# Kernel optimization log

Measured on AMD Instinct MI355X. Metric: run time of the kernel, lower is better.

The kernel has to match this reference:

```python
import jax, jax.numpy as jnp
import numpy as np

H = 16  # n_heads
D = 64  # d_keys


def setup_inputs() -> dict:
    key = jax.random.key(0)
    ks = jax.random.split(key, 11)
    b, n, dm = 2, 2048, 1024
    s = 1.0 / np.sqrt(dm)
    return {
        "q": jax.random.normal(ks[0], (b, n, dm), jnp.float32),
        "k": jax.random.normal(ks[1], (b, n, dm), jnp.float32),
        "v": jax.random.normal(ks[2], (b, n, dm), jnp.float32),
        "Wq": jax.random.normal(ks[3], (dm, H * D), jnp.float32) * s,
        "bq": jax.random.normal(ks[4], (H * D,), jnp.float32) * 0.01,
        "Wk": jax.random.normal(ks[5], (dm, H * D), jnp.float32) * s,
        "bk": jax.random.normal(ks[6], (H * D,), jnp.float32) * 0.01,
        "Wv": jax.random.normal(ks[7], (dm, H * D), jnp.float32) * s,
        "bv": jax.random.normal(ks[8], (H * D,), jnp.float32) * 0.01,
        "Wo": jax.random.normal(ks[9], (H * D, dm), jnp.float32) * s,
        "bo": jax.random.normal(ks[10], (dm,), jnp.float32) * 0.01,
    }


def reference(q, k, v, Wq, bq, Wk, bk, Wv, bv, Wo, bo):
    b, n_q, _ = q.shape
    n_k = k.shape[1]
    # projections -> [b, n, h, d]
    qh = (q @ Wq + bq).reshape(b, n_q, H, D)
    kh = (k @ Wk + bk).reshape(b, n_k, H, D)
    vh = (v @ Wv + bv).reshape(b, n_k, H, D)
    # scores [b, h, n, m]
    scores = jnp.einsum('bnhd,bmhd->bhnm', qh, kh)
    causal = jnp.triu(jnp.ones((n_q, n_k), dtype=bool), k=1)  # True above diag
    scores = jnp.where(causal, -jnp.inf, scores)
    att = jax.nn.softmax(scores / np.sqrt(D).astype(np.float32), axis=-1)
    att_out = jnp.einsum('bhnm,bmhd->bnhd', att, vh).reshape(b, n_q, H * D)
    return att_out @ Wo + bo
```

## Files before the change

kernel.cpp:

```cpp
#include <hip/hip_runtime.h>

typedef float f32x4 __attribute__((ext_vector_type(4)));
typedef __bf16 bf16x8 __attribute__((ext_vector_type(8)));
typedef __bf16 bf16x4 __attribute__((ext_vector_type(4)));
typedef __bf16 bf16_t;

#define NH 16
#define DH 64
#define SEQ 2048
#define DM 1024

#define QSCALE 0.18033688f

extern "C" hipError_t hipMemPtrGetInfo(void* ptr, size_t* size);

__device__ __forceinline__ bf16x8 ld8(const bf16_t* p) { return *(const bf16x8*)p; }
__device__ __forceinline__ void st8(bf16_t* p, bf16x8 v) { *(bf16x8*)p = v; }

__device__ __forceinline__ void gl_lds16(const bf16_t* g, bf16_t* l)
{
    __builtin_amdgcn_global_load_lds(
        (const __attribute__((address_space(1))) unsigned int*)g,
        (__attribute__((address_space(3))) unsigned int*)l, 16, 0, 0);
}

__global__ __launch_bounds__(256) void fill_sentinel(float* out, unsigned n, float val)
{
    unsigned stride = gridDim.x * blockDim.x;
    for (unsigned i = blockIdx.x * blockDim.x + threadIdx.x; i < n; i += stride)
        out[i] = val;
}

__global__ __launch_bounds__(256) void prep(
    const float* __restrict__ q, const float* __restrict__ k,
    const float* __restrict__ v,
    const float* __restrict__ w0, const float* __restrict__ w1,
    const float* __restrict__ w2, const float* __restrict__ w3,
    bf16_t* __restrict__ xb, bf16_t* __restrict__ wt, int fragmode)
{
    int z = blockIdx.z;
    if (z < 3) {
        const float* src = (z == 0) ? q : (z == 1) ? k : v;
        bf16_t* dst = xb + (size_t)z * (4096u * 1024u);
        size_t i8 = ((size_t)blockIdx.x * 256 + threadIdx.x) * 8;
        f32x4 u = *(const f32x4*)(src + i8);
        f32x4 w = *(const f32x4*)(src + i8 + 4);
        bf16x8 h = { (bf16_t)u.x, (bf16_t)u.y, (bf16_t)u.z, (bf16_t)u.w,
                     (bf16_t)w.x, (bf16_t)w.y, (bf16_t)w.z, (bf16_t)w.w };
        st8(dst + i8, h);
    } else {
        int x = blockIdx.x;
        if (x >= 1024) return;
        int w = x >> 8, rem = x & 255;
        int bx = rem & 15, by = rem >> 4;
        const float* in = (w == 0) ? w0 : (w == 1) ? w1 : (w == 2) ? w2 : w3;
        bf16_t* out = wt + (size_t)w * DM * DM;
        __shared__ __align__(16) bf16_t tile[64][72];
        int t = threadIdx.x;
        int k0 = by * 64, n0 = bx * 64;
        int r0 = t >> 4, c0 = (t & 15) * 4;
        for (int p = 0; p < 4; p++) {
            int r = r0 + p * 16;
            const float* src = in + (size_t)(k0 + r) * DM + n0 + c0;
            for (int i = 0; i < 4; i++) tile[r][c0 + i] = (bf16_t)src[i];
        }
        __syncthreads();
        if (fragmode && w < 3) {
            int idx = t;
            #pragma unroll
            for (int p = 0; p < 2; p++, idx += 256) {
                int rn = idx & 63;
                int kc8 = idx >> 6;
                int n_abs = n0 + rn;
                int rblk = n_abs >> 4, l16v = n_abs & 15;
                int kk = kc8 >> 2, gg = kc8 & 3;
                bf16x8 vv;
                for (int j = 0; j < 8; j++) vv[j] = tile[kc8 * 8 + j][rn];
                st8(out + (size_t)((rblk * 16 + by) * 2 + kk) * 512
                        + (gg * 16 + l16v) * 8, vv);
            }
        } else {
            for (int p = 0; p < 4; p++) {
                int rn = r0 + p * 16;
                bf16_t* dst = out + (size_t)(n0 + rn) * DM + k0 + c0;
                for (int i = 0; i < 4; i++) dst[i] = tile[c0 + i][rn];
            }
        }
    }
}

#define LGKM0 asm volatile("s_waitcnt lgkmcnt(0)" ::: "memory")
#define VMC(n) asm volatile("s_waitcnt vmcnt(" #n ")" ::: "memory")
#define BARRIER __builtin_amdgcn_s_barrier()

#define STA(d, h, dk) do { \
    _Pragma("unroll") for (int j = 0; j < 2; j++) \
        gl_lds16(Xp + ((h) * 128 + j * 64) * DM + (dk) * 64, \
                 Ab + sdst0 + ((d) * 2 + (h)) * 8192 + j * 4096); } while (0)
#define RDA(d, h, F) do { \
    _Pragma("unroll") for (int mf = 0; mf < 4; mf++) { \
        F[mf][0] = ld8(Ab + rA0 + ((d) * 2 + (h)) * 8192 + mf * 1024); \
        F[mf][1] = ld8(Ab + rA1 + ((d) * 2 + (h)) * 8192 + mf * 1024); } } while (0)
#define LDB(SET, nh, kto) do { \
    _Pragma("unroll") for (int nf = 0; nf < 2; nf++) \
        _Pragma("unroll") for (int kk = 0; kk < 2; kk++) \
            SET[nf][kk] = ld8(Bp + (nh) * 131072 + nf * 16384 \
                              + (kto) * 1024 + kk * 512); } while (0)
#define MMQ(AF, BF, Q) do { \
    __builtin_amdgcn_s_setprio(1); \
    _Pragma("unroll") for (int mf = 0; mf < 4; mf++) \
        _Pragma("unroll") for (int nf = 0; nf < 2; nf++) { \
            Q[mf][nf] = __builtin_amdgcn_mfma_f32_16x16x32_bf16( \
                AF[mf][0], BF[nf][0], Q[mf][nf], 0, 0, 0); \
            Q[mf][nf] = __builtin_amdgcn_mfma_f32_16x16x32_bf16( \
                AF[mf][1], BF[nf][1], Q[mf][nf], 0, 0, 0); } \
    __builtin_amdgcn_s_setprio(0); } while (0)

__global__ __launch_bounds__(512, 2) void gemm8(
    const bf16_t* __restrict__ xall, const bf16_t* __restrict__ bfall,
    const float* __restrict__ b0v, const float* __restrict__ b1v,
    const float* __restrict__ b2v, bf16_t* __restrict__ outall)
{
    int z = blockIdx.z;
    int mode = z;
    const bf16_t* X  = xall  + (size_t)z * (4096u * 1024u);
    const bf16_t* Bf = bfall + (size_t)z * (1024u * 1024u);
    const float* bias = (z == 0) ? b0v : (z == 1) ? b1v : b2v;
    bf16_t* out = outall + (size_t)z * (4096u * 1024u);

    int m0 = blockIdx.x * 256;
    int n0 = blockIdx.y * 256;

    __shared__ __align__(16) bf16_t Ab[2 * 2 * 128 * 64];

    int tid  = threadIdx.x;
    int lane = tid & 63, w = tid >> 6;
    int g = lane >> 4, l16 = lane & 15;
    int wm = w >> 2, wn = w & 3;
    int rl = lane >> 3, cl = lane & 7;
    int w8 = w * 8;

    int srow = w8 + rl;
    int scol = (cl ^ rl) * 8;
    const bf16_t* Xp = X + (size_t)(m0 + srow) * DM + scol;
    int sdst0 = w8 * 64 + lane * 8;

    int x7 = l16 & 7;
    int rA0 = (wm * 64 + l16) * 64 + ((0 + g) ^ x7) * 8;
    int rA1 = (wm * 64 + l16) * 64 + ((4 + g) ^ x7) * 8;

    const bf16_t* Bp = Bf + ((size_t)(n0 >> 4) + wn * 2) * 16384 + lane * 8;

    f32x4 a00[4][2] = {}, a01[4][2] = {}, a10[4][2] = {}, a11[4][2] = {};
    bf16x8 afA[4][2], afB[4][2], Ba[2][2], Bb[2][2];

    STA(0, 0, 0); STA(0, 1, 0); STA(1, 0, 1); STA(1, 1, 1);
    LDB(Ba, 0, 0); LDB(Bb, 1, 0);
    VMC(0);
    BARRIER;
    RDA(0, 0, afA);

    #pragma unroll 1
    for (int i = 0; i < 7; i++) {
        VMC(6); LGKM0; MMQ(afA, Ba, a00); BARRIER;
        STA(0, 0, 2); VMC(4); RDA(0, 1, afB); MMQ(afA, Bb, a01); BARRIER;
        LGKM0; MMQ(afB, Ba, a10); LDB(Ba, 0, 1); BARRIER;
        MMQ(afB, Bb, a11); LDB(Bb, 1, 1); STA(0, 1, 2); RDA(1, 0, afA); BARRIER;
        VMC(6); LGKM0; MMQ(afA, Ba, a00); BARRIER;
        STA(1, 0, 3); VMC(4); RDA(1, 1, afB); MMQ(afA, Bb, a01); BARRIER;
        LGKM0; MMQ(afB, Ba, a10); LDB(Ba, 0, 2); BARRIER;
        MMQ(afB, Bb, a11); LDB(Bb, 1, 2); STA(1, 1, 3); RDA(0, 0, afA); BARRIER;
        Xp += 128; Bp += 2048;
    }
    VMC(6); LGKM0; MMQ(afA, Ba, a00); BARRIER;
    VMC(2); RDA(0, 1, afB); MMQ(afA, Bb, a01); BARRIER;
    LGKM0; MMQ(afB, Ba, a10); LDB(Ba, 0, 1); BARRIER;
    MMQ(afB, Bb, a11); LDB(Bb, 1, 1); RDA(1, 0, afA); BARRIER;
    VMC(4); LGKM0; MMQ(afA, Ba, a00); BARRIER;
    VMC(0); RDA(1, 1, afB); MMQ(afA, Bb, a01); BARRIER;
    LGKM0; MMQ(afB, Ba, a10); BARRIER;
    MMQ(afB, Bb, a11);

    float scale = (mode == 0) ? QSCALE : 1.0f;
#define EPI(Q, Mh, Nh) do { \
    _Pragma("unroll") for (int mf = 0; mf < 4; mf++) { \
        int mbase = m0 + (Mh) * 128 + wm * 64 + mf * 16 + g * 4; \
        int bb = mbase >> 11, nn0 = mbase & 2047; \
        _Pragma("unroll") for (int nf = 0; nf < 2; nf++) { \
            int col = n0 + (Nh) * 128 + wn * 32 + nf * 16 + l16; \
            float bv = bias[col]; \
            int hh = col >> 6, dd = col & 63; \
            if (mode == 2) { \
                bf16x4 pv; \
                for (int r = 0; r < 4; r++) pv[r] = (bf16_t)(Q[mf][nf][r] + bv); \
                *(bf16x4*)(out + ((size_t)(bb * NH + hh) * DH + dd) * SEQ + nn0) = pv; \
            } else { \
                for (int r = 0; r < 4; r++) \
                    out[((size_t)(bb * NH + hh) * SEQ + nn0 + r) * DH + dd] = \
                        (bf16_t)((Q[mf][nf][r] + bv) * scale); \
            } } } } while (0)
    EPI(a00, 0, 0); EPI(a01, 0, 1); EPI(a10, 1, 0); EPI(a11, 1, 1);
#undef EPI
}

__global__ __launch_bounds__(256) void gemm_out(
    const bf16_t* __restrict__ X, const bf16_t* __restrict__ WT,
    const float* __restrict__ bias, bf16_t* __restrict__ out,
    float* __restrict__ outf, int out_is_f32)
{
    int m0 = blockIdx.x * 128;
    int n0 = blockIdx.y * 128;

    __shared__ __align__(16) bf16_t Alds[128 * 64];
    __shared__ __align__(16) bf16_t Blds[128 * 64];

    int t = threadIdx.x;
    int lane = t & 63, wave = t >> 6;
    int g = lane >> 4, l16 = lane & 15;
    int wr0 = (wave >> 1) * 64, wc0 = (wave & 1) * 64;
    int crow = lane >> 3;
    int ccol = (lane & 7) * 8;

    f32x4 acc[4][4] = {};

    for (int k0 = 0; k0 < DM; k0 += 64) {
        __syncthreads();
        for (int c = wave; c < 16; c += 4) {
            int row = c * 8 + crow;
            gl_lds16(X  + (size_t)(m0 + row) * DM + k0 + ccol,
                     Alds + c * 512 + lane * 8);
            gl_lds16(WT + (size_t)(n0 + row) * DM + k0 + ccol,
                     Blds + c * 512 + lane * 8);
        }
        __syncthreads();
        for (int kk = 0; kk < 2; kk++) {
            bf16x8 af[4], bfr[4];
            for (int i = 0; i < 4; i++)
                af[i] = ld8(Alds + (wr0 + i * 16 + l16) * 64 + kk * 32 + g * 8);
            for (int i = 0; i < 4; i++)
                bfr[i] = ld8(Blds + (wc0 + i * 16 + l16) * 64 + kk * 32 + g * 8);
            for (int mi = 0; mi < 4; mi++)
                for (int ni = 0; ni < 4; ni++)
                    acc[mi][ni] = __builtin_amdgcn_mfma_f32_16x16x32_bf16(
                        af[mi], bfr[ni], acc[mi][ni], 0, 0, 0);
        }
    }
    for (int mi = 0; mi < 4; mi++) {
        int mbase = m0 + wr0 + mi * 16 + g * 4;
        for (int ni = 0; ni < 4; ni++) {
            int col = n0 + wc0 + ni * 16 + l16;
            float bv = bias[col];
            for (int r = 0; r < 4; r++) {
                float sv = acc[mi][ni][r] + bv;
                if (out_is_f32) outf[(size_t)(mbase + r) * 1024 + col] = sv;
                else            out[(size_t)(mbase + r) * 1024 + col] = (bf16_t)sv;
            }
        }
    }
}

__global__ __launch_bounds__(256) void gemm_mha(
    const float* __restrict__ x0, const float* __restrict__ x1,
    const float* __restrict__ x2, const bf16_t* __restrict__ xb,
    const bf16_t* __restrict__ wt_base,
    const float* __restrict__ b0, const float* __restrict__ b1,
    const float* __restrict__ b2, bf16_t* __restrict__ out_base,
    float* __restrict__ outf, int mode_base, int out_is_f32)
{
    int z = blockIdx.z;
    const float* Xf    = (z == 0) ? x0 : (z == 1) ? x1 : x2;
    const bf16_t* WT   = wt_base + (size_t)z * DM * DM;
    const float* bias  = (z == 0) ? b0 : (z == 1) ? b1 : b2;
    bf16_t* out = out_base + (size_t)z * (4096u * 1024u);
    int mode = mode_base + z;

    int m0 = blockIdx.x * 128;
    int n0 = blockIdx.y * 128;

    __shared__ __align__(16) bf16_t Alds[128 * 64];
    __shared__ __align__(16) bf16_t Blds[128 * 64];

    int t = threadIdx.x;
    int lane = t & 63, wave = t >> 6;
    int g = lane >> 4, l16 = lane & 15;
    int wr0 = (wave >> 1) * 64, wc0 = (wave & 1) * 64;

    f32x4 acc[4][4] = {};
    int srow = t >> 3, sk = (t & 7) * 8;

    for (int k0 = 0; k0 < DM; k0 += 64) {
        __syncthreads();
        if (mode < 3) {
            for (int p = 0; p < 4; p++) {
                int r = srow + p * 32;
                const float* s4 = Xf + (size_t)(m0 + r) * DM + k0 + sk;
                f32x4 u = *(const f32x4*)s4;
                f32x4 w = *(const f32x4*)(s4 + 4);
                bf16x8 h = { (bf16_t)u.x, (bf16_t)u.y, (bf16_t)u.z, (bf16_t)u.w,
                             (bf16_t)w.x, (bf16_t)w.y, (bf16_t)w.z, (bf16_t)w.w };
                st8(Alds + r * 64 + sk, h);
            }
        } else {
            for (int p = 0; p < 4; p++) {
                int r = srow + p * 32;
                st8(Alds + r * 64 + sk, ld8(xb + (size_t)(m0 + r) * DM + k0 + sk));
            }
        }
        for (int p = 0; p < 4; p++) {
            int r = srow + p * 32;
            st8(Blds + r * 64 + sk, ld8(WT + (size_t)(n0 + r) * DM + k0 + sk));
        }
        __syncthreads();
        for (int kk = 0; kk < 2; kk++) {
            bf16x8 af[4], bfr[4];
            for (int i = 0; i < 4; i++)
                af[i] = ld8(Alds + (wr0 + i * 16 + l16) * 64 + kk * 32 + g * 8);
            for (int i = 0; i < 4; i++)
                bfr[i] = ld8(Blds + (wc0 + i * 16 + l16) * 64 + kk * 32 + g * 8);
            for (int mi = 0; mi < 4; mi++)
                for (int ni = 0; ni < 4; ni++)
                    acc[mi][ni] = __builtin_amdgcn_mfma_f32_16x16x32_bf16(
                        af[mi], bfr[ni], acc[mi][ni], 0, 0, 0);
        }
    }
    float scale = (mode == 0) ? QSCALE : 1.0f;
    for (int mi = 0; mi < 4; mi++) {
        int mbase = m0 + wr0 + mi * 16 + g * 4;
        for (int ni = 0; ni < 4; ni++) {
            int col = n0 + wc0 + ni * 16 + l16;
            float bv = bias[col];
            if (mode == 2) {
                int bb = mbase >> 11, nn0 = mbase & 2047;
                int h = col >> 6, d = col & 63;
                bf16x4 pv;
                for (int r = 0; r < 4; r++) pv[r] = (bf16_t)(acc[mi][ni][r] + bv);
                *(bf16x4*)(out + ((size_t)(bb * NH + h) * DH + d) * SEQ + nn0) = pv;
            } else {
                for (int r = 0; r < 4; r++) {
                    int mr = mbase + r;
                    float sv = (acc[mi][ni][r] + bv) * scale;
                    if (mode == 3) {
                        if (out_is_f32) outf[(size_t)mr * 1024 + col] = sv;
                        else            out[(size_t)mr * 1024 + col] = (bf16_t)sv;
                    } else {
                        int bb = mr >> 11, nn = mr & 2047;
                        int h = col >> 6, d = col & 63;
                        out[((size_t)(bb * NH + h) * SEQ + nn) * DH + d] = (bf16_t)sv;
                    }
                }
            }
        }
    }
}

__constant__ unsigned char JP[24] = {7,15,15,14,14,6,13,13,12,12,5,11,
                                     11,10,10,4,9,9,8,8,3,2,1,0};
__constant__ unsigned char JS[24] = {0,0,1,0,1,0,0,1,0,1,0,0,
                                     1,0,1,0,0,1,0,1,0,0,0,0};

__global__ __launch_bounds__(512) void attn_split(
    const bf16_t* __restrict__ Qh, const bf16_t* __restrict__ Kh,
    const bf16_t* __restrict__ VT, bf16_t* __restrict__ att,
    float* __restrict__ Pb, float* __restrict__ Lb)
{
    int bhx = blockIdx.x;
    int y   = blockIdx.y;
    int p   = JP[y];
    int seg = JS[y];
    bool splitf = (p >= 8);
    int k0 = splitf ? seg * (p + 1) : 0;
    int k1 = splitf ? k0 + (p + 1) : 2 * p + 2;

    const bf16_t* Qb = Qh + (size_t)bhx * SEQ * DH;
    const bf16_t* Kb = Kh + (size_t)bhx * SEQ * DH;
    const bf16_t* Vb = VT + (size_t)bhx * DH * SEQ;

    __shared__ __align__(16) bf16_t Klds[64 * 72];
    __shared__ __align__(16) bf16_t Vlds[64 * 72];
    __shared__ __align__(16) bf16_t Plds[8][16 * 72];

    int t = threadIdx.x, lane = t & 63, wave = t >> 6;
    int g = lane >> 4, l16 = lane & 15;
    int srow = t >> 3, sk = (t & 7) * 8;
    int qt = 2 * p + (wave >> 2);
    int Tw = qt + 1;
    int rowl = (wave & 3) * 16 + l16;

    bf16x8 qf[2];
    for (int kk = 0; kk < 2; kk++)
        qf[kk] = ld8(Qb + (size_t)(qt * 64 + rowl) * DH + kk * 32 + g * 8);

    f32x4 accO[4] = {};
    float l = 0.f;
    bf16_t* Pw = Plds[wave];

    bf16x8 kreg = ld8(Kb + (size_t)(k0 * 64 + srow) * DH + sk);
    bf16x8 vreg = ld8(Vb + (size_t)srow * SEQ + k0 * 64 + sk);
    st8(&Klds[srow * 72 + sk], kreg);
    if (k0 + 1 < k1)
        kreg = ld8(Kb + (size_t)((k0 + 1) * 64 + srow) * DH + sk);

    for (int j = k0; j < k1; j++) {
        __syncthreads();
        st8(&Vlds[srow * 72 + sk], vreg);
        if (j + 1 < k1)
            vreg = ld8(Vb + (size_t)srow * SEQ + (j + 1) * 64 + sk);

        bool act  = (j < Tw);
        bool diag = (j == Tw - 1);
        if (act) {
            f32x4 s[4];
            __builtin_amdgcn_s_setprio(1);
            for (int c = 0; c < 4; c++) {
                f32x4 a = {};
                for (int kk = 0; kk < 2; kk++) {
                    bf16x8 kf = ld8(&Klds[(c * 16 + l16) * 72 + kk * 32 + g * 8]);
                    a = __builtin_amdgcn_mfma_f32_16x16x32_bf16(kf, qf[kk], a, 0, 0, 0);
                }
                s[c] = a;
            }
            __builtin_amdgcn_s_setprio(0);
            for (int c = 0; c < 4; c++) {
                bf16x4 pv;
                for (int r = 0; r < 4; r++) {
                    float v = s[c][r];
                    if (diag && (c * 16 + g * 4 + r) > rowl) v = -1e30f;
                    float pe;
                    asm("v_exp_f32 %0, %1" : "=v"(pe) : "v"(v));
                    l += pe;
                    pv[r] = (bf16_t)pe;
                }
                *(bf16x4*)(Pw + l16 * 72 + c * 16 + g * 4) = pv;
            }
        }
        __syncthreads();
        if (j + 1 < k1) {
            st8(&Klds[srow * 72 + sk], kreg);
            if (j + 2 < k1)
                kreg = ld8(Kb + (size_t)((j + 2) * 64 + srow) * DH + sk);
        }
        if (act) {
            bf16x8 pf0 = ld8(Pw + l16 * 72 + g * 8);
            bf16x8 pf1 = ld8(Pw + l16 * 72 + 32 + g * 8);
            __builtin_amdgcn_s_setprio(1);
            for (int c2 = 0; c2 < 4; c2++) {
                bf16x8 vf0 = ld8(&Vlds[(c2 * 16 + l16) * 72 + g * 8]);
                accO[c2] = __builtin_amdgcn_mfma_f32_16x16x32_bf16(vf0, pf0, accO[c2], 0, 0, 0);
                bf16x8 vf1 = ld8(&Vlds[(c2 * 16 + l16) * 72 + 32 + g * 8]);
                accO[c2] = __builtin_amdgcn_mfma_f32_16x16x32_bf16(vf1, pf1, accO[c2], 0, 0, 0);
            }
            __builtin_amdgcn_s_setprio(0);

            if (diag && !splitf) {
                float lt = l;
                lt += __shfl_xor(lt, 16);
                lt += __shfl_xor(lt, 32);
                float inv = 1.f / lt;
                int qabs = qt * 64 + rowl;
                int bb = bhx >> 4, h = bhx & 15;
                for (int c2 = 0; c2 < 4; c2++) {
                    bf16x4 ov;
                    for (int r = 0; r < 4; r++) ov[r] = (bf16_t)(accO[c2][r] * inv);
                    *(bf16x4*)(att + (((size_t)bb * SEQ + qabs) * NH + h) * DH
                               + c2 * 16 + g * 4) = ov;
                }
            }
        }
    }

    if (splitf) {
        float lt = l;
        lt += __shfl_xor(lt, 16);
        lt += __shfl_xor(lt, 32);
        int slot = (bhx * 16 + (qt - 16)) * 2 + seg;
        float* Pp = Pb + (size_t)slot * 4096 + rowl * 64;
        #pragma unroll
        for (int c2 = 0; c2 < 4; c2++)
            *(f32x4*)(Pp + c2 * 16 + g * 4) = accO[c2];
        if (g == 0) Lb[slot * 64 + rowl] = lt;
    }
}

__global__ __launch_bounds__(256) void attn_combine(
    const float* __restrict__ Pb, const float* __restrict__ Lb,
    bf16_t* __restrict__ att)
{
    int bhx = blockIdx.x, q16 = blockIdx.y;
    int qt = 16 + q16;
    int t = threadIdx.x;
    int row = t >> 2, dc = (t & 3) * 16;

    int slot0 = (bhx * 16 + q16) * 2;
    int slot1 = slot0 + 1;
    float lsum = Lb[slot0 * 64 + row] + Lb[slot1 * 64 + row];
    float inv = 1.f / lsum;

    const float* P0 = Pb + (size_t)slot0 * 4096 + row * 64 + dc;
    const float* P1 = Pb + (size_t)slot1 * 4096 + row * 64 + dc;
    int qabs = qt * 64 + row;
    int bb = bhx >> 4, h = bhx & 15;
    bf16_t* ob = att + (((size_t)bb * SEQ + qabs) * NH + h) * DH + dc;
    #pragma unroll
    for (int c = 0; c < 4; c++) {
        f32x4 a = *(const f32x4*)(P0 + c * 4);
        f32x4 b = *(const f32x4*)(P1 + c * 4);
        bf16x4 ov;
        for (int r = 0; r < 4; r++) ov[r] = (bf16_t)((a[r] + b[r]) * inv);
        *(bf16x4*)(ob + c * 4) = ov;
    }
}

__global__ __launch_bounds__(512) void attn(
    const bf16_t* __restrict__ Qh, const bf16_t* __restrict__ Kh,
    const bf16_t* __restrict__ VT, bf16_t* __restrict__ att)
{
    int bhx = blockIdx.x;
    int yy  = blockIdx.y;
    int p   = (yy < 8) ? yy : 23 - yy;
    int TB  = 2 * p + 2;

    const bf16_t* Qb = Qh + (size_t)bhx * SEQ * DH;
    const bf16_t* Kb = Kh + (size_t)bhx * SEQ * DH;
    const bf16_t* Vb = VT + (size_t)bhx * DH * SEQ;

    __shared__ __align__(16) bf16_t Klds[2][64 * 72];
    __shared__ __align__(16) bf16_t Vlds[2][64 * 72];
    __shared__ __align__(16) bf16_t Plds[8][16 * 72];

    int t = threadIdx.x, lane = t & 63, wave = t >> 6;
    int g = lane >> 4, l16 = lane & 15;
    int srow = t >> 3, sk = (t & 7) * 8;
    int qt = 2 * p + (wave >> 2);
    int Tw = qt + 1;
    int rowl = (wave & 3) * 16 + l16;

    bf16x8 qf[2];
    for (int kk = 0; kk < 2; kk++)
        qf[kk] = ld8(Qb + (size_t)(qt * 64 + rowl) * DH + kk * 32 + g * 8);

    f32x4 accO[4] = {};
    float l = 0.f;
    bf16_t* Pw = Plds[wave];

    st8(&Klds[0][srow * 72 + sk], ld8(Kb + (size_t)srow * DH + sk));
    st8(&Vlds[0][srow * 72 + sk], ld8(Vb + (size_t)srow * SEQ + sk));

    for (int j = 0; j < TB; j++) {
        __syncthreads();
        bool pre = (j + 1 < TB);
        bf16x8 kreg, vreg;
        if (pre) {
            kreg = ld8(Kb + (size_t)((j + 1) * 64 + srow) * DH + sk);
            vreg = ld8(Vb + (size_t)srow * SEQ + (j + 1) * 64 + sk);
        }
        if (j < Tw) {
            int buf = j & 1;
            bool diag = (j == Tw - 1);

            f32x4 s[4];
            __builtin_amdgcn_s_setprio(1);
            for (int c = 0; c < 4; c++) {
                f32x4 a = {};
                for (int kk = 0; kk < 2; kk++) {
                    bf16x8 kf = ld8(&Klds[buf][(c * 16 + l16) * 72 + kk * 32 + g * 8]);
                    a = __builtin_amdgcn_mfma_f32_16x16x32_bf16(kf, qf[kk], a, 0, 0, 0);
                }
                s[c] = a;
            }
            __builtin_amdgcn_s_setprio(0);
            for (int c = 0; c < 4; c++) {
                bf16x4 pv;
                for (int r = 0; r < 4; r++) {
                    float v = s[c][r];
                    if (diag && (c * 16 + g * 4 + r) > rowl) v = -1e30f;
                    float pe;
                    asm("v_exp_f32 %0, %1" : "=v"(pe) : "v"(v));
                    l += pe;
                    pv[r] = (bf16_t)pe;
                }
                *(bf16x4*)(Pw + l16 * 72 + c * 16 + g * 4) = pv;
            }
            asm volatile("s_waitcnt lgkmcnt(0)" ::: "memory");

            bf16x8 pf0 = ld8(Pw + l16 * 72 + g * 8);
            bf16x8 pf1 = ld8(Pw + l16 * 72 + 32 + g * 8);
            __builtin_amdgcn_s_setprio(1);
            for (int c2 = 0; c2 < 4; c2++) {
                bf16x8 vf0 = ld8(&Vlds[buf][(c2 * 16 + l16) * 72 + g * 8]);
                accO[c2] = __builtin_amdgcn_mfma_f32_16x16x32_bf16(vf0, pf0, accO[c2], 0, 0, 0);
                bf16x8 vf1 = ld8(&Vlds[buf][(c2 * 16 + l16) * 72 + 32 + g * 8]);
                accO[c2] = __builtin_amdgcn_mfma_f32_16x16x32_bf16(vf1, pf1, accO[c2], 0, 0, 0);
            }
            __builtin_amdgcn_s_setprio(0);

            if (diag) {
                float lt = l;
                lt += __shfl_xor(lt, 16);
                lt += __shfl_xor(lt, 32);
                float inv = 1.f / lt;
                int qabs = qt * 64 + rowl;
                int bb = bhx >> 4, h = bhx & 15;
                for (int c2 = 0; c2 < 4; c2++) {
                    bf16x4 ov;
                    for (int r = 0; r < 4; r++) ov[r] = (bf16_t)(accO[c2][r] * inv);
                    *(bf16x4*)(att + (((size_t)bb * SEQ + qabs) * NH + h) * DH
                               + c2 * 16 + g * 4) = ov;
                }
            }
        }
        if (pre) {
            int b = (j + 1) & 1;
            st8(&Klds[b][srow * 72 + sk], kreg);
            st8(&Vlds[b][srow * 72 + sk], vreg);
        }
    }
}

extern "C" void kernel_launch(void* const* d_in, const int* in_sizes, int n_in,
                              void* d_out, int out_size, void* d_ws, size_t ws_size,
                              hipStream_t stream) {
    const float* q  = (const float*)d_in[0];
    const float* k  = (const float*)d_in[1];
    const float* v  = (const float*)d_in[2];
    const float* Wq = (const float*)d_in[3];
    const float* bq = (const float*)d_in[4];
    const float* Wk = (const float*)d_in[5];
    const float* bk = (const float*)d_in[6];
    const float* Wv = (const float*)d_in[7];
    const float* bv = (const float*)d_in[8];
    const float* Wo = (const float*)d_in[9];
    const float* bo = (const float*)d_in[10];

    const size_t MAT = 1024u * 1024u;
    const size_t BIG = 4096u * 1024u;
    const size_t NEED_BASE = 64 + (4 * BIG + 4 * MAT) * 2;
    const size_t NEED_FAST = NEED_BASE + 3 * BIG * 2;

    if (ws_size < NEED_BASE) {
        fill_sentinel<<<1024, 256, 0, stream>>>((float*)d_out,
                                                (unsigned)out_size, 100.0f);
        return;
    }

    int out_is_f32 = 1;
    size_t osz = 0;
    if (hipMemPtrGetInfo(d_out, &osz) == hipSuccess && osz != 0 &&
        osz < (size_t)out_size * 4)
        out_is_f32 = 0;

    bf16_t* base = (bf16_t*)d_ws + 32;
    bf16_t* Qh  = base;
    bf16_t* Kh  = Qh + BIG;
    bf16_t* VT  = Kh + BIG;
    bf16_t* att = VT + BIG;
    bf16_t* WT  = att + BIG;
    bf16_t* Xb  = WT + 4 * MAT;

    if (ws_size >= NEED_FAST) {
        float* Pb = (float*)Xb;
        float* Lb = Pb + (size_t)1024 * 4096;
        prep<<<dim3(2048, 1, 4), 256, 0, stream>>>(q, k, v, Wq, Wk, Wv, Wo,
                                                   Xb, WT, 1);
        gemm8<<<dim3(16, 4, 3), 512, 0, stream>>>(Xb, WT, bq, bk, bv, Qh);
        attn_split<<<dim3(32, 24), 512, 0, stream>>>(Qh, Kh, VT, att, Pb, Lb);
        attn_combine<<<dim3(32, 16), 256, 0, stream>>>(Pb, Lb, att);
        gemm_out<<<dim3(32, 8), 256, 0, stream>>>(att, WT + 3 * MAT, bo,
                                                  (bf16_t*)d_out, (float*)d_out,
                                                  out_is_f32);
    } else {
        prep<<<dim3(2048, 1, 4), 256, 0, stream>>>(q, k, v, Wq, Wk, Wv, Wo,
                                                   (bf16_t*)d_ws, WT, 0);
        gemm_mha<<<dim3(32, 8, 3), 256, 0, stream>>>(q, k, v, nullptr, WT,
                                                     bq, bk, bv, Qh, nullptr, 0, 0);
        attn<<<dim3(32, 16), 512, 0, stream>>>(Qh, Kh, VT, att);
        gemm_mha<<<dim3(32, 8, 1), 256, 0, stream>>>(nullptr, nullptr, nullptr, att,
                                                     WT + 3 * MAT, bo, bo, bo,
                                                     (bf16_t*)d_out, (float*)d_out,
                                                     3, out_is_f32);
    }
}
```

Measured before the change: 225.9 us.

## Remap QKV GEMM waves to 64x128 subtiles with four B fragment sets

Changes the 8-wave decomposition of the 256x256 QKV projection tile from 2x4 waves (each covering two M halves and two N halves) to 4x2 waves, each owning 64 rows and 128 contiguous columns. Each wave now reads only one A half from LDS per k-step and streams four B fragment sets straight from global memory, with the software pipeline and vmcnt waits reworked to match. The aim is to cut LDS A-fragment reads and re-sync stalls in exchange for more direct global B traffic and more registers for B fragments, which could hurt occupancy at two blocks per CU.

Measured after the change: 268.5 us. +18.9%, slower.

```diff
diff --git a/kernel.cpp b/kernel.cpp
--- a/kernel.cpp
+++ b/kernel.cpp
@@ -97,14 +97,14 @@
     _Pragma("unroll") for (int j = 0; j < 2; j++) \
         gl_lds16(Xp + ((h) * 128 + j * 64) * DM + (dk) * 64, \
                  Ab + sdst0 + ((d) * 2 + (h)) * 8192 + j * 4096); } while (0)
-#define RDA(d, h, F) do { \
+#define RDA2(d, F) do { \
     _Pragma("unroll") for (int mf = 0; mf < 4; mf++) { \
-        F[mf][0] = ld8(Ab + rA0 + ((d) * 2 + (h)) * 8192 + mf * 1024); \
-        F[mf][1] = ld8(Ab + rA1 + ((d) * 2 + (h)) * 8192 + mf * 1024); } } while (0)
-#define LDB(SET, nh, kto) do { \
+        F[mf][0] = ld8(Ab + rA0 + ((d) * 2 + hw) * 8192 + mf * 1024); \
+        F[mf][1] = ld8(Ab + rA1 + ((d) * 2 + hw) * 8192 + mf * 1024); } } while (0)
+#define LDB2(SET, q, kto) do { \
     _Pragma("unroll") for (int nf = 0; nf < 2; nf++) \
         _Pragma("unroll") for (int kk = 0; kk < 2; kk++) \
-            SET[nf][kk] = ld8(Bp + (nh) * 131072 + nf * 16384 \
+            SET[nf][kk] = ld8(Bp + ((q) * 2 + nf) * 16384 \
                               + (kto) * 1024 + kk * 512); } while (0)
 #define MMQ(AF, BF, Q) do { \
     __builtin_amdgcn_s_setprio(1); \
@@ -136,7 +136,9 @@
     int tid  = threadIdx.x;
     int lane = tid & 63, w = tid >> 6;
     int g = lane >> 4, l16 = lane & 15;
-    int wm = w >> 2, wn = w & 3;
+    int wm = w >> 1, wn = w & 1;
+    int hw = w >> 2;
+    int rb = (wm & 1) * 64;
     int rl = lane >> 3, cl = lane & 7;
     int w8 = w * 8;
 
@@ -146,48 +148,64 @@
     int sdst0 = w8 * 64 + lane * 8;
 
     int x7 = l16 & 7;
-    int rA0 = (wm * 64 + l16) * 64 + ((0 + g) ^ x7) * 8;
-    int rA1 = (wm * 64 + l16) * 64 + ((4 + g) ^ x7) * 8;
-
-    const bf16_t* Bp = Bf + ((size_t)(n0 >> 4) + wn * 2) * 16384 + lane * 8;
-
-    f32x4 a00[4][2] = {}, a01[4][2] = {}, a10[4][2] = {}, a11[4][2] = {};
-    bf16x8 afA[4][2], afB[4][2], Ba[2][2], Bb[2][2];
+    int rA0 = (rb + l16) * 64 + ((0 + g) ^ x7) * 8;
+    int rA1 = (rb + l16) * 64 + ((4 + g) ^ x7) * 8;
+
+    const bf16_t* Bp = Bf + ((size_t)(n0 >> 4) + wn * 8) * 16384 + lane * 8;
+
+    f32x4 a0[4][2] = {}, a1[4][2] = {}, a2[4][2] = {}, a3[4][2] = {};
+    bf16x8 afA[4][2], afB[4][2];
+    bf16x8 Bs0[2][2], Bs1[2][2], Bs2[2][2], Bs3[2][2];
 
     STA(0, 0, 0); STA(0, 1, 0); STA(1, 0, 1); STA(1, 1, 1);
-    LDB(Ba, 0, 0); LDB(Bb, 1, 0);
+    LDB2(Bs0, 0, 0); LDB2(Bs1, 1, 0); LDB2(Bs2, 2, 0); LDB2(Bs3, 3, 0);
     VMC(0);
     BARRIER;
-    RDA(0, 0, afA);
+    RDA2(0, afA);
 
     #pragma unroll 1
     for (int i = 0; i < 7; i++) {
-        VMC(6); LGKM0; MMQ(afA, Ba, a00); BARRIER;
-        STA(0, 0, 2); VMC(4); RDA(0, 1, afB); MMQ(afA, Bb, a01); BARRIER;
-        LGKM0; MMQ(afB, Ba, a10); LDB(Ba, 0, 1); BARRIER;
-        MMQ(afB, Bb, a11); LDB(Bb, 1, 1); STA(0, 1, 2); RDA(1, 0, afA); BARRIER;
-        VMC(6); LGKM0; MMQ(afA, Ba, a00); BARRIER;
-        STA(1, 0, 3); VMC(4); RDA(1, 1, afB); MMQ(afA, Bb, a01); BARRIER;
-        LGKM0; MMQ(afB, Ba, a10); LDB(Ba, 0, 2); BARRIER;
-        MMQ(afB, Bb, a11); LDB(Bb, 1, 2); STA(1, 1, 3); RDA(0, 0, afA); BARRIER;
+        VMC(8); LGKM0;
+        MMQ(afA, Bs0, a0); LDB2(Bs0, 0, 1); BARRIER;
+        STA(0, 0, 2);
+        MMQ(afA, Bs1, a1); LDB2(Bs1, 1, 1); BARRIER;
+        VMC(14); STA(0, 1, 2);
+        MMQ(afA, Bs2, a2); LDB2(Bs2, 2, 1); BARRIER;
+        VMC(16); RDA2(1, afB);
+        MMQ(afA, Bs3, a3); LDB2(Bs3, 3, 1); BARRIER;
+        VMC(16); LGKM0;
+        MMQ(afB, Bs0, a0); LDB2(Bs0, 0, 2); BARRIER;
+        VMC(14); STA(1, 0, 3);
+        MMQ(afB, Bs1, a1); LDB2(Bs1, 1, 2); BARRIER;
+        VMC(14); STA(1, 1, 3);
+        MMQ(afB, Bs2, a2); LDB2(Bs2, 2, 2); BARRIER;
+        VMC(16); RDA2(0, afA);
+        MMQ(afB, Bs3, a3); LDB2(Bs3, 3, 2); BARRIER;
         Xp += 128; Bp += 2048;
     }
-    VMC(6); LGKM0; MMQ(afA, Ba, a00); BARRIER;
-    VMC(2); RDA(0, 1, afB); MMQ(afA, Bb, a01); BARRIER;
-    LGKM0; MMQ(afB, Ba, a10); LDB(Ba, 0, 1); BARRIER;
-    MMQ(afB, Bb, a11); LDB(Bb, 1, 1); RDA(1, 0, afA); BARRIER;
-    VMC(4); LGKM0; MMQ(afA, Ba, a00); BARRIER;
-    VMC(0); RDA(1, 1, afB); MMQ(afA, Bb, a01); BARRIER;
-    LGKM0; MMQ(afB, Ba, a10); BARRIER;
-    MMQ(afB, Bb, a11);
+    VMC(8); LGKM0;
+    MMQ(afA, Bs0, a0); LDB2(Bs0, 0, 1); BARRIER;
+    MMQ(afA, Bs1, a1); LDB2(Bs1, 1, 1); BARRIER;
+    VMC(12);
+    MMQ(afA, Bs2, a2); LDB2(Bs2, 2, 1); BARRIER;
+    VMC(12); RDA2(1, afB);
+    MMQ(afA, Bs3, a3); LDB2(Bs3, 3, 1); BARRIER;
+    VMC(12); LGKM0;
+    MMQ(afB, Bs0, a0); BARRIER;
+    VMC(8);
+    MMQ(afB, Bs1, a1); BARRIER;
+    VMC(4);
+    MMQ(afB, Bs2, a2); BARRIER;
+    VMC(0);
+    MMQ(afB, Bs3, a3);
 
     float scale = (mode == 0) ? QSCALE : 1.0f;
-#define EPI(Q, Mh, Nh) do { \
+#define EPI2(Q, q) do { \
     _Pragma("unroll") for (int mf = 0; mf < 4; mf++) { \
-        int mbase = m0 + (Mh) * 128 + wm * 64 + mf * 16 + g * 4; \
+        int mbase = m0 + wm * 64 + mf * 16 + g * 4; \
         int bb = mbase >> 11, nn0 = mbase & 2047; \
         _Pragma("unroll") for (int nf = 0; nf < 2; nf++) { \
-            int col = n0 + (Nh) * 128 + wn * 32 + nf * 16 + l16; \
+            int col = n0 + wn * 128 + (q) * 32 + nf * 16 + l16; \
             float bv = bias[col]; \
             int hh = col >> 6, dd = col & 63; \
             if (mode == 2) { \
@@ -199,8 +217,8 @@
                     out[((size_t)(bb * NH + hh) * SEQ + nn0 + r) * DH + dd] = \
                         (bf16_t)((Q[mf][nf][r] + bv) * scale); \
             } } } } while (0)
-    EPI(a00, 0, 0); EPI(a01, 0, 1); EPI(a10, 1, 0); EPI(a11, 1, 1);
-#undef EPI
+    EPI2(a0, 0); EPI2(a1, 1); EPI2(a2, 2); EPI2(a3, 3);
+#undef EPI2
 }
 
 __global__ __launch_bounds__(256) void gemm_out(
```
